# Optimization experiments

Hardware: AMD Instinct MI355X
Metric: run time of the kernel (lower is better)

## Reference

```python
import jax, jax.numpy as jnp
import numpy as np

NUM_EMBEDDINGS = 1024
EMBEDDING_DIM = 256

def setup_inputs() -> dict:
    key = jax.random.key(0)
    k1, k2 = jax.random.split(key)
    z_e = jax.random.normal(k1, (32, 256, 64, 64), dtype=jnp.float32)
    # nn.Embedding weight init uniform_(-1/K, 1/K)
    lim = 1.0 / NUM_EMBEDDINGS
    codebook = jax.random.uniform(k2, (NUM_EMBEDDINGS, EMBEDDING_DIM), dtype=jnp.float32,
                                  minval=-lim, maxval=lim)
    return {"z_e": z_e, "codebook": codebook}

def reference(z_e, codebook):
    B, C, H, W = z_e.shape
    # [B,C,H,W] -> [B*H*W, C]
    z_flat = jnp.transpose(z_e, (0, 2, 3, 1)).reshape(-1, C)
    # squared L2 distances: ||z||^2 + ||e||^2 - 2 z.e  -> [N, K]
    distances = (jnp.sum(z_flat ** 2, axis=1, keepdims=True)
                 + jnp.sum(codebook ** 2, axis=1)
                 - 2.0 * jnp.matmul(z_flat, codebook.T))
    encoding_indices = jnp.argmin(distances, axis=1)  # [N]
    z_q = codebook[encoding_indices].reshape(B, H, W, C)
    z_q = jnp.transpose(z_q, (0, 3, 1, 2))  # [B,C,H,W]
    sg = jax.lax.stop_gradient
    codebook_loss = jnp.mean((sg(z_q) - z_e) ** 2)
    commitment_loss = jnp.mean((sg(z_e) - z_q) ** 2)
    return z_q, codebook_loss + 0.25 * commitment_loss, encoding_indices
```

## Files before the change

kernel.cpp:

```cpp
#include <hip/hip_runtime.h>
#include <stdint.h>

typedef __attribute__((ext_vector_type(8))) _Float16 half8;
typedef __attribute__((ext_vector_type(4))) float f32x4;

#define CDIM 256
#define KCODES 1024
#define NPTS 131072
#define ZQ_ELEMS 33554432u
#define CAP 32768
#define MARGIN 3.0e-4f

#define WS_IMG 0
#define WS_S2 (16 * 65536)
#define WS_IDX (WS_S2 + 4096)
#define WS_PART (WS_IDX + NPTS * 4)
#define WS_CNT (WS_PART + 65536)
#define WS_LIST (WS_CNT + 64)

__device__ __forceinline__ float np_pairwise_sq_256(const float* x) {
    float res[2];
#pragma unroll
    for (int h = 0; h < 2; h++) {
        const float* a = x + h * 128;
        float r[8];
#pragma unroll
        for (int j = 0; j < 8; j++) r[j] = __fmul_rn(a[j], a[j]);
#pragma unroll
        for (int i = 8; i < 128; i += 8)
#pragma unroll
            for (int j = 0; j < 8; j++)
                r[j] = __fadd_rn(r[j], __fmul_rn(a[i + j], a[i + j]));
        res[h] = __fadd_rn(__fadd_rn(__fadd_rn(r[0], r[1]), __fadd_rn(r[2], r[3])),
                           __fadd_rn(__fadd_rn(r[4], r[5]), __fadd_rn(r[6], r[7])));
    }
    return __fadd_rn(res[0], res[1]);
}

__global__ __launch_bounds__(256) void vq_prep(const float* __restrict__ cb,
                                               unsigned char* __restrict__ img,
                                               int* __restrict__ cnt) {
    int t = threadIdx.x;
    if (blockIdx.x == 0 && t == 0) *cnt = 0;
    int codeLocal = t >> 5;
    int cg = t & 31;
    int k = blockIdx.x * 8 + codeLocal;
    const float* row = cb + k * CDIM + cg * 8;
    union H { _Float16 h[8]; uint4 u; } hi;
#pragma unroll
    for (int j = 0; j < 8; j++) hi.h[j] = (_Float16)(row[j] * 1024.f);
    int chunk = k >> 5, rowi = k & 31;
    int ks = cg >> 2, l4 = cg & 3;
    int q = rowi >> 4, l15 = rowi & 15;
    int lane = l4 * 16 + l15;
    *(uint4*)(img + chunk * 16384 + ((ks * 2 + q) << 10) + lane * 16) = hi.u;
}

__global__ __launch_bounds__(256) void vq_s2prep(const float* __restrict__ cb,
                                                 float* __restrict__ s2) {
    int k = blockIdx.x * 256 + threadIdx.x;
    float e[256];
#pragma unroll
    for (int c = 0; c < 256; c++) e[c] = cb[(size_t)k * CDIM + c];
    s2[k] = np_pairwise_sq_256(e);
}

__global__ __launch_bounds__(256, 2) void vq_dist(const float* __restrict__ z,
                                                  const unsigned char* __restrict__ img,
                                                  const float* __restrict__ s2g,
                                                  int* __restrict__ outIdx,
                                                  int* __restrict__ cnt,
                                                  int* __restrict__ list) {
    __shared__ __align__(16) unsigned char smem[3][16384];
    __shared__ float e2s[1024];
    int t = threadIdx.x;
    int lane = t & 63, wave = t >> 6;
    int l15 = lane & 15, l4 = lane >> 4;
    int blk0 = blockIdx.x * 256;
    int wbase = blk0 + wave * 64;
    int b = blk0 >> 12;
    int hwb0 = blk0 & 4095;
    const float* zb = z + (size_t)b * (CDIM * 4096);
    unsigned char* sbase = &smem[0][0];

#pragma unroll
    for (int i = 0; i < 4; i++) e2s[t + i * 256] = s2g[t + i * 256];

    half8 aHi[4][8];
#pragma unroll
    for (int ks = 0; ks < 8; ks++) {
        __syncthreads();
#pragma unroll
        for (int i = 0; i < 8; i++) {
            int u = i * 256 + t;
            int row = u >> 6, col16 = u & 63;
            const float* gsrc = zb + (size_t)(ks * 32 + row) * 4096 + hwb0 + col16 * 4;
            __builtin_amdgcn_global_load_lds(
                (const __attribute__((address_space(1))) void*)gsrc,
                (__attribute__((address_space(3))) void*)(sbase + (size_t)u * 16), 16, 0, 0);
        }
        __syncthreads();
#pragma unroll
        for (int m = 0; m < 4; m++) {
            half8 h;
#pragma unroll
            for (int j = 0; j < 8; j++) {
                float f = *(const float*)(sbase +
                        (size_t)(((l4 * 8 + j) << 8) + wave * 64 + m * 16 + l15) * 4) * 32.f;
                h[j] = (_Float16)f;
            }
            aHi[m][ks] = h;
        }
    }
    __syncthreads();

#pragma unroll
    for (int i = 0; i < 4; i++) {
        size_t off = (size_t)(i * 256 + t) * 16;
        __builtin_amdgcn_global_load_lds(
            (const __attribute__((address_space(1))) void*)(img + off),
            (__attribute__((address_space(3))) void*)(&smem[0][0] + off), 16, 0, 0);
    }
#pragma unroll
    for (int i = 0; i < 4; i++) {
        size_t off = (size_t)(i * 256 + t) * 16;
        __builtin_amdgcn_global_load_lds(
            (const __attribute__((address_space(1))) void*)(img + 16384 + off),
            (__attribute__((address_space(3))) void*)(&smem[1][0] + off), 16, 0, 0);
    }

    float bestv[4][4], bestv2[4][4];
    int besti[4][4];
#pragma unroll
    for (int m = 0; m < 4; m++)
#pragma unroll
        for (int j = 0; j < 4; j++) { bestv[m][j] = 3.0e38f; bestv2[m][j] = 3.0e38f; besti[m][j] = 0; }

    int i0 = 0, i1 = 1, i2 = 2;
    for (int chunk = 0; chunk < 32; chunk++) {
        if (chunk < 31) asm volatile("s_waitcnt vmcnt(4)" ::: "memory");
        else            asm volatile("s_waitcnt vmcnt(0)" ::: "memory");
        __builtin_amdgcn_s_barrier();

        if (chunk + 2 < 32) {
            const unsigned char* src = img + (size_t)(chunk + 2) * 16384;
            unsigned char* dst = &smem[0][0] + (size_t)i2 * 16384;
#pragma unroll
            for (int i = 0; i < 4; i++) {
                size_t off = (size_t)(i * 256 + t) * 16;
                __builtin_amdgcn_global_load_lds(
                    (const __attribute__((address_space(1))) void*)(src + off),
                    (__attribute__((address_space(3))) void*)(dst + off), 16, 0, 0);
            }
        }

        f32x4 acc[4][2];
#pragma unroll
        for (int m = 0; m < 4; m++)
#pragma unroll
            for (int q = 0; q < 2; q++) acc[m][q] = (f32x4){0.f, 0.f, 0.f, 0.f};

        const unsigned char* bufc = &smem[0][0] + (size_t)i0 * 16384 + lane * 16;
#pragma unroll
        for (int ks = 0; ks < 8; ks++) {
            half8 b0 = *(const half8*)(bufc + (ks << 11));
            half8 b1 = *(const half8*)(bufc + (ks << 11) + 1024);
#pragma unroll
            for (int m = 0; m < 4; m++) {
                acc[m][0] = __builtin_amdgcn_mfma_f32_16x16x32_f16(aHi[m][ks], b0, acc[m][0], 0, 0, 0);
                acc[m][1] = __builtin_amdgcn_mfma_f32_16x16x32_f16(aHi[m][ks], b1, acc[m][1], 0, 0, 0);
            }
        }
#pragma unroll
        for (int q = 0; q < 2; q++) {
            int code = chunk * 32 + q * 16 + l15;
            float ev = e2s[code];
#pragma unroll
            for (int m = 0; m < 4; m++)
#pragma unroll
                for (int j = 0; j < 4; j++) {
                    float s = fmaf(acc[m][q][j], -6.103515625e-05f, ev);
                    if (s < bestv[m][j]) { bestv2[m][j] = bestv[m][j]; bestv[m][j] = s; besti[m][j] = code; }
                    else if (s < bestv2[m][j]) bestv2[m][j] = s;
                }
        }
        int tmp = i0; i0 = i1; i1 = i2; i2 = tmp;
    }

#pragma unroll
    for (int m = 0; m < 4; m++)
#pragma unroll
        for (int j = 0; j < 4; j++) {
            float v = bestv[m][j], v2 = bestv2[m][j];
            int idx = besti[m][j];
#pragma unroll
            for (int off = 1; off < 16; off <<= 1) {
                float ov = __shfl_xor(v, off);
                float ov2 = __shfl_xor(v2, off);
                int oi = __shfl_xor(idx, off);
                if (ov < v || (ov == v && oi < idx)) { v2 = fminf(v, ov2); v = ov; idx = oi; }
                else v2 = fminf(v2, ov);
            }
            if (l15 == 0) {
                int p = wbase + m * 16 + l4 * 4 + j;
                outIdx[p] = idx;
                if (v2 - v < MARGIN) {
                    int pos = atomicAdd(cnt, 1);
                    if (pos < CAP) list[pos] = p;
                }
            }
        }
}

__global__ __launch_bounds__(256) void vq_cbt(const float* __restrict__ cb,
                                              float* __restrict__ cbT) {
    int k = blockIdx.x * 256 + threadIdx.x;
    for (int c = 0; c < 256; c++) cbT[c * 1024 + k] = cb[(size_t)k * 256 + c];
}

__global__ __launch_bounds__(256) void vq_rescue(const float* __restrict__ z,
                                                 const float* __restrict__ cbT,
                                                 const float* __restrict__ s2,
                                                 const int* __restrict__ list,
                                                 const int* __restrict__ cnt,
                                                 int* __restrict__ outIdx) {
    __shared__ float zs[8][256];
    __shared__ float S1s[8];
    __shared__ float rv[256];
    __shared__ int ri[256];
    int n = *cnt; if (n > CAP) n = CAP;
    int t = threadIdx.x;
    for (int base = blockIdx.x * 8; base < n; base += gridDim.x * 8) {
        int npts = n - base; if (npts > 8) npts = 8;
        __syncthreads();
        {
            int pp = t >> 5, c0 = (t & 31) * 8;
            if (pp < npts) {
                int p = list[base + pp];
                int b = p >> 12, hw = p & 4095;
                const float* zp = z + ((size_t)b << 20) + hw;
#pragma unroll
                for (int j = 0; j < 8; j++) zs[pp][c0 + j] = zp[(size_t)(c0 + j) << 12];
            }
        }
        __syncthreads();
        if (t < npts) S1s[t] = np_pairwise_sq_256(zs[t]);
        __syncthreads();

        float d[8][4];
#pragma unroll
        for (int pp = 0; pp < 8; pp++)
#pragma unroll
            for (int q = 0; q < 4; q++) d[pp][q] = 0.f;
        for (int c = 0; c < 256; c++) {
            const float* er = cbT + c * 1024 + t;
            float e0 = er[0], e1 = er[256], e2v = er[512], e3 = er[768];
#pragma unroll
            for (int pp = 0; pp < 8; pp++) {
                float zc = zs[pp][c];
                d[pp][0] = fmaf(zc, e0, d[pp][0]);
                d[pp][1] = fmaf(zc, e1, d[pp][1]);
                d[pp][2] = fmaf(zc, e2v, d[pp][2]);
                d[pp][3] = fmaf(zc, e3, d[pp][3]);
            }
        }
        float s2v[4] = {s2[t], s2[256 + t], s2[512 + t], s2[768 + t]};

        float bv[8]; int bi[8];
#pragma unroll
        for (int pp = 0; pp < 8; pp++) {
            float v = 3.4e38f; int i0 = 0;
#pragma unroll
            for (int q = 0; q < 4; q++) {
                float dist = __fsub_rn(__fadd_rn(S1s[pp], s2v[q]), __fmul_rn(2.0f, d[pp][q]));
                if (dist < v) { v = dist; i0 = q * 256 + t; }
            }
            bv[pp] = v; bi[pp] = i0;
        }
        for (int pp = 0; pp < 8; pp++) {
            if (pp >= npts) break;
            rv[t] = bv[pp]; ri[t] = bi[pp];
            __syncthreads();
            for (int sft = 128; sft > 0; sft >>= 1) {
                if (t < sft) {
                    if (rv[t + sft] < rv[t] || (rv[t + sft] == rv[t] && ri[t + sft] < ri[t])) {
                        rv[t] = rv[t + sft]; ri[t] = ri[t + sft];
                    }
                }
                __syncthreads();
            }
            if (t == 0) outIdx[list[base + pp]] = ri[0];
            __syncthreads();
        }
    }
}

__global__ __launch_bounds__(256) void vq_gather(const float* __restrict__ z,
                                                 const float* __restrict__ cb,
                                                 const int* __restrict__ idxs,
                                                 float* __restrict__ out,
                                                 float* __restrict__ partial) {
    int unit = blockIdx.x * 256 + threadIdx.x;
    int hw4 = unit & 1023;
    int cgb = unit >> 10;
    int b = cgb >> 5, cg = cgb & 31;

    int4 ids = *(const int4*)&idxs[(b << 12) + hw4 * 4];
    float va[4][8];
#pragma unroll
    for (int e = 0; e < 4; e++) {
        int id = (e == 0) ? ids.x : (e == 1) ? ids.y : (e == 2) ? ids.z : ids.w;
        const float4* cr = (const float4*)(cb + (size_t)id * CDIM + cg * 8);
        float4 v0 = cr[0], v1 = cr[1];
        va[e][0] = v0.x; va[e][1] = v0.y; va[e][2] = v0.z; va[e][3] = v0.w;
        va[e][4] = v1.x; va[e][5] = v1.y; va[e][6] = v1.z; va[e][7] = v1.w;
    }

    float s = 0.f;
#pragma unroll
    for (int j = 0; j < 8; j++) {
        size_t addr = (((size_t)(b * 256 + cg * 8 + j)) << 12) + hw4 * 4;
        float4 zv = *(const float4*)&z[addr];
        float4 ov = {va[0][j], va[1][j], va[2][j], va[3][j]};
        *(float4*)&out[addr] = ov;
        float d0 = ov.x - zv.x, d1 = ov.y - zv.y, d2 = ov.z - zv.z, d3 = ov.w - zv.w;
        s = fmaf(d0, d0, s); s = fmaf(d1, d1, s);
        s = fmaf(d2, d2, s); s = fmaf(d3, d3, s);
    }
    if (cg == 0) {
        size_t ib = (size_t)ZQ_ELEMS + 1u + (b << 12) + hw4 * 4;
        out[ib + 0] = (float)ids.x;
        out[ib + 1] = (float)ids.y;
        out[ib + 2] = (float)ids.z;
        out[ib + 3] = (float)ids.w;
    }
#pragma unroll
    for (int off = 32; off > 0; off >>= 1) s += __shfl_down(s, off);
    __shared__ float red[4];
    if ((threadIdx.x & 63) == 0) red[threadIdx.x >> 6] = s;
    __syncthreads();
    if (threadIdx.x == 0) partial[blockIdx.x] = red[0] + red[1] + red[2] + red[3];
}

__global__ __launch_bounds__(512) void vq_finalize(const float* __restrict__ partial,
                                                   float* __restrict__ out) {
    int t = threadIdx.x;
    double s = 0.0;
    for (int i = t; i < 4096; i += 512) s += (double)partial[i];
#pragma unroll
    for (int off = 32; off > 0; off >>= 1) s += __shfl_down(s, off);
    __shared__ double sd[8];
    if ((t & 63) == 0) sd[t >> 6] = s;
    __syncthreads();
    if (t == 0) {
        double tot = sd[0] + sd[1] + sd[2] + sd[3] + sd[4] + sd[5] + sd[6] + sd[7];
        out[ZQ_ELEMS] = (float)(1.25 * tot / (double)ZQ_ELEMS);
    }
}

extern "C" void kernel_launch(void* const* d_in, const int* in_sizes, int n_in,
                              void* d_out, int out_size, void* d_ws, size_t ws_size,
                              hipStream_t stream) {
    const float* z = (const float*)d_in[0];
    const float* cb = (const float*)d_in[1];
    unsigned char* ws = (unsigned char*)d_ws;
    unsigned char* img = ws + WS_IMG;
    float* cbT = (float*)(ws + WS_IMG);
    float* s2 = (float*)(ws + WS_S2);
    int* idx = (int*)(ws + WS_IDX);
    float* partial = (float*)(ws + WS_PART);
    int* cnt = (int*)(ws + WS_CNT);
    int* list = (int*)(ws + WS_LIST);
    float* out = (float*)d_out;

    vq_prep<<<128, 256, 0, stream>>>(cb, img, cnt);
    vq_s2prep<<<4, 256, 0, stream>>>(cb, s2);
    vq_dist<<<512, 256, 0, stream>>>(z, img, s2, idx, cnt, list);
    vq_cbt<<<4, 256, 0, stream>>>(cb, cbT);
    vq_rescue<<<512, 256, 0, stream>>>(z, cbT, s2, list, cnt, idx);
    vq_gather<<<4096, 256, 0, stream>>>(z, cb, idx, out, partial);
    vq_finalize<<<1, 512, 0, stream>>>(partial, out);
}
```

Measured before the change: 359.5 us.

## Compute the loss from the expanded distance in vq_dist and drop the z re-read in gather

Each point's squared error is rewritten as ||z||^2 plus the minimum expanded distance. ||z||^2 is accumulated while vq_dist converts z to fp16, so per-block loss partials come out of vq_dist and vq_gather no longer reads z. This removes a full pass over the large input in the gather kernel. The trade-off is that the loss now uses the fp16-approximated distance and ignores index changes made by the rescue kernel, which slightly shifts precision. Separately, the codebook-norm prep is spread over more blocks, staging rows through shared memory with coalesced loads.

```diff
diff --git a/kernel.cpp b/kernel.cpp
--- a/kernel.cpp
+++ b/kernel.cpp
@@ -58,11 +58,19 @@
 
 __global__ __launch_bounds__(256) void vq_s2prep(const float* __restrict__ cb,
                                                  float* __restrict__ s2) {
-    int k = blockIdx.x * 256 + threadIdx.x;
-    float e[256];
-#pragma unroll
-    for (int c = 0; c < 256; c++) e[c] = cb[(size_t)k * CDIM + c];
-    s2[k] = np_pairwise_sq_256(e);
+    __shared__ float rows[32 * 261];
+    int t = threadIdx.x;
+    int k0 = blockIdx.x * 32;
+#pragma unroll
+    for (int i = 0; i < 8; i++) {
+        int u = i * 256 + t;
+        int row = u >> 6, c4 = u & 63;
+        float4 v = *(const float4*)&cb[(size_t)(k0 + row) * CDIM + c4 * 4];
+        float* d = &rows[row * 261 + c4 * 4];
+        d[0] = v.x; d[1] = v.y; d[2] = v.z; d[3] = v.w;
+    }
+    __syncthreads();
+    if (t < 32) s2[k0 + t] = np_pairwise_sq_256(&rows[t * 261]);
 }
 
 __global__ __launch_bounds__(256, 2) void vq_dist(const float* __restrict__ z,
@@ -70,9 +78,11 @@
                                                   const float* __restrict__ s2g,
                                                   int* __restrict__ outIdx,
                                                   int* __restrict__ cnt,
-                                                  int* __restrict__ list) {
+                                                  int* __restrict__ list,
+                                                  float* __restrict__ partial) {
     __shared__ __align__(16) unsigned char smem[3][16384];
     __shared__ float e2s[1024];
+    __shared__ float lred[4];
     int t = threadIdx.x;
     int lane = t & 63, wave = t >> 6;
     int l15 = lane & 15, l4 = lane >> 4;
@@ -87,6 +97,7 @@
     for (int i = 0; i < 4; i++) e2s[t + i * 256] = s2g[t + i * 256];
 
     half8 aHi[4][8];
+    float s1p[4] = {0.f, 0.f, 0.f, 0.f};
 #pragma unroll
     for (int ks = 0; ks < 8; ks++) {
         __syncthreads();
@@ -103,16 +114,24 @@
 #pragma unroll
         for (int m = 0; m < 4; m++) {
             half8 h;
+            float ss = s1p[m];
 #pragma unroll
             for (int j = 0; j < 8; j++) {
                 float f = *(const float*)(sbase +
                         (size_t)(((l4 * 8 + j) << 8) + wave * 64 + m * 16 + l15) * 4) * 32.f;
                 h[j] = (_Float16)f;
+                ss = fmaf(f, f, ss);
             }
             aHi[m][ks] = h;
+            s1p[m] = ss;
         }
     }
     __syncthreads();
+#pragma unroll
+    for (int m = 0; m < 4; m++) {
+        s1p[m] += __shfl_xor(s1p[m], 16);
+        s1p[m] += __shfl_xor(s1p[m], 32);
+    }
 
 #pragma unroll
     for (int i = 0; i < 4; i++) {
@@ -187,6 +206,7 @@
         int tmp = i0; i0 = i1; i1 = i2; i2 = tmp;
     }
 
+    float lsum = 0.f;
 #pragma unroll
     for (int m = 0; m < 4; m++)
 #pragma unroll
@@ -201,7 +221,10 @@
                 if (ov < v || (ov == v && oi < idx)) { v2 = fminf(v, ov2); v = ov; idx = oi; }
                 else v2 = fminf(v2, ov);
             }
+            int r = l4 * 4 + j;
+            float S1r = __shfl(s1p[m], r) * 9.765625e-4f;
             if (l15 == 0) {
+                lsum += S1r + v;
                 int p = wbase + m * 16 + l4 * 4 + j;
                 outIdx[p] = idx;
                 if (v2 - v < MARGIN) {
@@ -210,6 +233,11 @@
                 }
             }
         }
+#pragma unroll
+    for (int off = 32; off > 0; off >>= 1) lsum += __shfl_down(lsum, off);
+    if (lane == 0) lred[wave] = lsum;
+    __syncthreads();
+    if (t == 0) partial[blockIdx.x] = lred[0] + lred[1] + lred[2] + lred[3];
 }
 
 __global__ __launch_bounds__(256) void vq_cbt(const float* __restrict__ cb,
@@ -295,11 +323,9 @@
     }
 }
 
-__global__ __launch_bounds__(256) void vq_gather(const float* __restrict__ z,
-                                                 const float* __restrict__ cb,
+__global__ __launch_bounds__(256) void vq_gather(const float* __restrict__ cb,
                                                  const int* __restrict__ idxs,
-                                                 float* __restrict__ out,
-                                                 float* __restrict__ partial) {
+                                                 float* __restrict__ out) {
     int unit = blockIdx.x * 256 + threadIdx.x;
     int hw4 = unit & 1023;
     int cgb = unit >> 10;
@@ -315,17 +341,11 @@
         va[e][0] = v0.x; va[e][1] = v0.y; va[e][2] = v0.z; va[e][3] = v0.w;
         va[e][4] = v1.x; va[e][5] = v1.y; va[e][6] = v1.z; va[e][7] = v1.w;
     }
-
-    float s = 0.f;
 #pragma unroll
     for (int j = 0; j < 8; j++) {
         size_t addr = (((size_t)(b * 256 + cg * 8 + j)) << 12) + hw4 * 4;
-        float4 zv = *(const float4*)&z[addr];
         float4 ov = {va[0][j], va[1][j], va[2][j], va[3][j]};
         *(float4*)&out[addr] = ov;
-        float d0 = ov.x - zv.x, d1 = ov.y - zv.y, d2 = ov.z - zv.z, d3 = ov.w - zv.w;
-        s = fmaf(d0, d0, s); s = fmaf(d1, d1, s);
-        s = fmaf(d2, d2, s); s = fmaf(d3, d3, s);
     }
     if (cg == 0) {
         size_t ib = (size_t)ZQ_ELEMS + 1u + (b << 12) + hw4 * 4;
@@ -334,19 +354,12 @@
         out[ib + 2] = (float)ids.z;
         out[ib + 3] = (float)ids.w;
     }
-#pragma unroll
-    for (int off = 32; off > 0; off >>= 1) s += __shfl_down(s, off);
-    __shared__ float red[4];
-    if ((threadIdx.x & 63) == 0) red[threadIdx.x >> 6] = s;
-    __syncthreads();
-    if (threadIdx.x == 0) partial[blockIdx.x] = red[0] + red[1] + red[2] + red[3];
 }
 
 __global__ __launch_bounds__(512) void vq_finalize(const float* __restrict__ partial,
                                                    float* __restrict__ out) {
     int t = threadIdx.x;
-    double s = 0.0;
-    for (int i = t; i < 4096; i += 512) s += (double)partial[i];
+    double s = (t < 512) ? (double)partial[t] : 0.0;
 #pragma unroll
     for (int off = 32; off > 0; off >>= 1) s += __shfl_down(s, off);
     __shared__ double sd[8];
@@ -374,10 +387,10 @@
     float* out = (float*)d_out;
 
     vq_prep<<<128, 256, 0, stream>>>(cb, img, cnt);
-    vq_s2prep<<<4, 256, 0, stream>>>(cb, s2);
-    vq_dist<<<512, 256, 0, stream>>>(z, img, s2, idx, cnt, list);
+    vq_s2prep<<<32, 256, 0, stream>>>(cb, s2);
+    vq_dist<<<512, 256, 0, stream>>>(z, img, s2, idx, cnt, list, partial);
     vq_cbt<<<4, 256, 0, stream>>>(cb, cbT);
     vq_rescue<<<512, 256, 0, stream>>>(z, cbT, s2, list, cnt, idx);
-    vq_gather<<<4096, 256, 0, stream>>>(z, cb, idx, out, partial);
+    vq_gather<<<4096, 256, 0, stream>>>(cb, idx, out);
     vq_finalize<<<1, 512, 0, stream>>>(partial, out);
 }
```

Measured after the change: 335.1 us. -6.8%, faster.
